# Optimization experiments

Measured on AMD Instinct MI355X. Metric: run time of the kernel, lower is better.

Reference implementation:

```python
import jax, jax.numpy as jnp
import numpy as np

N, E, D, M, R, NH, HD, FF = 20000, 160000, 64, 4, 5, 4, 16, 16


def _ln(x, g, b, eps=1e-5):
    mu = x.mean(-1, keepdims=True)
    var = ((x - mu) ** 2).mean(-1, keepdims=True)
    return (x - mu) / jnp.sqrt(var + eps) * g + b


def _encoder(x, p):
    # Post-norm nn.TransformerEncoderLayer(D, nhead=4, dim_feedforward=16), eval mode.
    # x: (B, 4, D); returns CLS output (B, D). Padding mask is all-zeros -> no masking.
    B = x.shape[0]
    qkv = x @ p['in_w'].T + p['in_b']                     # (B,4,3D)
    q, k, v = jnp.split(qkv, 3, axis=-1)
    hview = lambda t: t.reshape(B, 4, NH, HD).transpose(0, 2, 1, 3)  # (B,H,4,hd)
    q, k, v = hview(q), hview(k), hview(v)
    attn = jax.nn.softmax(jnp.einsum('bhqd,bhkd->bhqk', q, k) / jnp.sqrt(jnp.float32(HD)), axis=-1)
    o = jnp.einsum('bhqk,bhkd->bhqd', attn, v).transpose(0, 2, 1, 3).reshape(B, 4, D)
    o = o @ p['out_w'].T + p['out_b']
    x = _ln(x + o, p['ln1_g'], p['ln1_b'])
    ff = jax.nn.relu(x @ p['ff1_w'].T + p['ff1_b']) @ p['ff2_w'].T + p['ff2_b']
    x = _ln(x + ff, p['ln2_g'], p['ln2_b'])
    return x[:, 0, :]


def _mem_encode(h_a, h_b, cls_w, sep, p):
    # For each memory slot m: encode [CLS_m, h_a, SEP, h_b]; sum CLS outputs.
    B = h_a.shape[0]
    sep_t = jnp.broadcast_to(sep, (B, 1, D))
    outs = []
    mem_emb = jnp.zeros((B, D), h_a.dtype)
    for m in range(M):  # small fixed loop over memory slots
        cls_t = jnp.broadcast_to(cls_w[m], (B, 1, D))
        seq = jnp.concatenate([cls_t, h_a[:, None, :], sep_t, h_b[:, None, :]], axis=1)
        t = _encoder(seq, p)
        outs.append(t)
        mem_emb = mem_emb + t
    return mem_emb, outs


def setup_inputs() -> dict:
    key = jax.random.key(0)
    ks = jax.random.split(key, 16)
    s = 0.05
    f32 = jnp.float32
    inp = {}
    inp['feat'] = jax.random.normal(ks[0], (N, D), f32)
    inp['src'] = jax.random.randint(ks[1], (E,), 0, N, dtype=jnp.int32)
    inp['dst'] = jax.random.randint(ks[2], (E,), 0, N, dtype=jnp.int32)
    inp['etype'] = jax.random.randint(ks[3], (E,), 0, R, dtype=jnp.int32)
    inp['cls_w'] = jax.random.normal(ks[4], (M, D), f32)           # CLS embedding, std=1 as in source
    inp['sep'] = jax.random.normal(ks[5], (D,), f32)
    inp['in_w'] = jax.random.normal(ks[6], (3 * D, D), f32) * s
    inp['in_b'] = jnp.zeros((3 * D,), f32)
    inp['out_w'] = jax.random.normal(ks[7], (D, D), f32) * s
    inp['out_b'] = jnp.zeros((D,), f32)
    inp['ln1_g'] = jnp.ones((D,), f32)
    inp['ln1_b'] = jnp.zeros((D,), f32)
    inp['ln2_g'] = jnp.ones((D,), f32)
    inp['ln2_b'] = jnp.zeros((D,), f32)
    inp['ff1_w'] = jax.random.normal(ks[8], (FF, D), f32) * s
    inp['ff1_b'] = jnp.zeros((FF,), f32)
    inp['ff2_w'] = jax.random.normal(ks[9], (D, FF), f32) * s
    inp['ff2_b'] = jnp.zeros((D,), f32)
    inp['memcat_w'] = jax.random.normal(ks[10], (M, D), f32) * s
    inp['memcat_b'] = jnp.zeros((M,), f32)
    inp['memw_w'] = jax.random.normal(ks[11], (D * D, D), f32) * s
    inp['h_bias'] = jnp.zeros((D,), f32)
    inp['lnw_g'] = jnp.ones((D,), f32)
    inp['lnw_b'] = jnp.zeros((D,), f32)
    return inp


def reference(feat, src, dst, etype, cls_w, sep, in_w, in_b, out_w, out_b,
              ln1_g, ln1_b, ln2_g, ln2_b, ff1_w, ff1_b, ff2_w, ff2_b,
              memcat_w, memcat_b, memw_w, h_bias, lnw_g, lnw_b):
    p = dict(in_w=in_w, in_b=in_b, out_w=out_w, out_b=out_b, ln1_g=ln1_g, ln1_b=ln1_b,
             ln2_g=ln2_g, ln2_b=ln2_b, ff1_w=ff1_w, ff1_b=ff1_b, ff2_w=ff2_w, ff2_b=ff2_b)
    h_src = feat[src]                                      # (E,D) gather
    h_dst = feat[dst]
    # Per-etype loop in the source uses identical params for every edge, so the message
    # math vectorizes over all edges; only category/label ordering depends on etype.
    mem_emb, outs = _mem_encode(h_src, h_dst, cls_w, sep, p)   # (E,D)
    cat_all = jnp.stack([t @ memcat_w.T + memcat_b for t in outs])  # (M,E,mem_size)
    # Reproduce source ordering: for etype e (ascending), for slot m, edges in original order.
    counts = jnp.bincount(etype, length=R)
    start = jnp.cumsum(counts) - counts                    # exclusive prefix
    perm = jnp.argsort(etype)                              # stable sort by etype
    e_s = etype[perm]
    local = jnp.arange(E) - start[e_s]
    pos = M * start[e_s][None, :] + jnp.arange(M)[:, None] * counts[e_s][None, :] + local[None, :]  # (M,E)
    category = jnp.zeros((M * E, M), cat_all.dtype).at[pos.reshape(-1)].set(cat_all[:, perm].reshape(M * E, M))
    label = jnp.zeros((M * E,), jnp.int32).at[pos.reshape(-1)].set(
        jnp.broadcast_to(jnp.arange(M, dtype=jnp.int32)[:, None], (M, E)).reshape(-1))
    # Dynamic per-edge weight + message
    w = (mem_emb @ memw_w.T).reshape(-1, D, D)             # (E, out, in)
    msg = jnp.einsum('eoi,ei->eo', w, h_src)               # (E,D)
    # fn.mean aggregation (zero-degree nodes -> 0, matching DGL)
    deg = jax.ops.segment_sum(jnp.ones((E,), feat.dtype), dst, num_segments=N)
    agg = jax.ops.segment_sum(msg, dst, num_segments=N) / jnp.maximum(deg, 1.0)[:, None]
    node = _ln(agg, lnw_g, lnw_b) + h_bias
    # self-loop branch: same memory-slot transformer on (feat, feat)
    mem_emb_n, _ = _mem_encode(feat, feat, cls_w, sep, p)
    w_n = (mem_emb_n @ memw_w.T).reshape(-1, D, D)
    node = node + jnp.einsum('noi,ni->no', w_n, feat)
    node = jnp.where(node > 0, node, 0.2 * node)           # LeakyReLU(0.2); dropout is identity in eval
    return node, category, label
```

## Files before the change

kernel.cpp:

```cpp
#include <hip/hip_runtime.h>

#define DI __device__ __forceinline__

static constexpr int NN = 20000;
static constexpr int NE = 160000;

typedef __attribute__((ext_vector_type(4))) float f32x4;
typedef _Float16 f16x2 __attribute__((ext_vector_type(2)));
typedef _Float16 f16x8 __attribute__((ext_vector_type(8)));

DI float rl(float v, int lane) {
    return __int_as_float(__builtin_amdgcn_readlane(__float_as_int(v), lane));
}
DI float xr(float v, int m) { return __shfl_xor(v, m, 64); }
DI int xri(int v, int m) { return __shfl_xor(v, m, 64); }
DI float wsum64(float v) {
    v += xr(v, 1); v += xr(v, 2); v += xr(v, 4);
    v += xr(v, 8); v += xr(v, 16); v += xr(v, 32);
    return v;
}
DI int wsum64i(int v) {
    v += xri(v, 1); v += xri(v, 2); v += xri(v, 4);
    v += xri(v, 8); v += xri(v, 16); v += xri(v, 32);
    return v;
}
DI float hsum16(float v) {
    v += xr(v, 1); v += xr(v, 2); v += xr(v, 4); v += xr(v, 8);
    return v;
}
DI float hsum16d(float v) {
    v += __int_as_float(__builtin_amdgcn_mov_dpp(__float_as_int(v), 0xB1, 0xF, 0xF, true));
    v += __int_as_float(__builtin_amdgcn_mov_dpp(__float_as_int(v), 0x4E, 0xF, 0xF, true));
    v += __int_as_float(__builtin_amdgcn_mov_dpp(__float_as_int(v), 0x141, 0xF, 0xF, true));
    v += __int_as_float(__builtin_amdgcn_mov_dpp(__float_as_int(v), 0x140, 0xF, 0xF, true));
    return v;
}
DI float wsum64v(float v) {
    v = hsum16d(v);
    return (rl(v, 0) + rl(v, 16)) + (rl(v, 32) + rl(v, 48));
}
DI unsigned short f2h(float x) {
    union { _Float16 f; unsigned short u; } c;
    c.f = (_Float16)x;
    return c.u;
}

__global__ __launch_bounds__(256) void prepA_kernel(
    const float* __restrict__ mw, unsigned short* __restrict__ Wstg,
    const float* __restrict__ in_w, const float* __restrict__ out_w,
    float* __restrict__ WOVg,
    const float* __restrict__ cls_w, const float* __restrict__ sep,
    const float* __restrict__ in_b,
    const int* __restrict__ et, int* __restrict__ bc,
    float* __restrict__ agg, float* __restrict__ deg,
    const float* __restrict__ mc_w, const float* __restrict__ mc_b,
    const float* __restrict__ ln1_g, const float* __restrict__ ln1_b,
    const float* __restrict__ ln2_g, const float* __restrict__ ln2_b,
    const float* __restrict__ ff1_w, const float* __restrict__ ff1_b,
    const float* __restrict__ out_b,
    float* __restrict__ SWg, float* __restrict__ SB16,
    float* __restrict__ OvcG, float* __restrict__ OvsG,
    float* __restrict__ bOvG, float* __restrict__ s0n,
    float* __restrict__ s2n, float* __restrict__ MC8,
    float* __restrict__ GcT, float* __restrict__ GsT,
    float* __restrict__ DCC, float* __restrict__ B0T,
    float* __restrict__ mgT) {
    int b = blockIdx.x, t = threadIdx.x;
    __shared__ int c[5];
    __shared__ float P[608];
    if (b < 1024) {
        int idx = b * 256 + t;
        int d = idx & 63, o = (idx >> 6) & 63, i = idx >> 12;
        Wstg[idx] = f2h(mw[(o * 64 + i) * 64 + d]);
    } else if (b < 1088) {
        int u = (b - 1024) * 256 + t;
        int h = u & 3, l = (u >> 2) & 63, j = u >> 8;
        float acc = 0.f;
        for (int i = 0; i < 16; i++)
            acc += out_w[l * 64 + h * 16 + i] * in_w[(128 + h * 16 + i) * 64 + j];
        WOVg[u] = acc;
    } else if (b == 1088) {
        if (t < 64) {
            int l = t;
            float bq = in_b[l], bk = in_b[64 + l], bv = in_b[128 + l];
            float xs = sep[l];
            float ks = bk, vs = bv;
            for (int j = 0; j < 64; j++) {
                float xj = rl(xs, j);
                ks += in_w[(64 + l) * 64 + j] * xj;
                vs += in_w[(128 + l) * 64 + j] * xj;
            }
            P[512 + l] = vs;
            for (int m = 0; m < 4; m++) {
                float xc = cls_w[m * 64 + l];
                float q0 = bq, kc = bk, vc = bv;
                for (int j = 0; j < 64; j++) {
                    float xj = rl(xc, j);
                    q0 += in_w[l * 64 + j] * xj;
                    kc += in_w[(64 + l) * 64 + j] * xj;
                    vc += in_w[(128 + l) * 64 + j] * xj;
                }
                P[m * 64 + l] = q0;
                P[256 + m * 64 + l] = vc;
                float p0 = hsum16(q0 * kc);
                float p2 = hsum16(q0 * ks);
                if ((l & 15) == 0) {
                    P[576 + m * 4 + (l >> 4)] = p0 * 0.25f;
                    P[592 + m * 4 + (l >> 4)] = p2 * 0.25f;
                }
            }
        }
        __syncthreads();
        for (int u = t; u < 1024; u += 256) {
            int m = u >> 8, h = (u >> 6) & 3, j = u & 63;
            float acc = 0.f;
            for (int i = 0; i < 16; i++)
                acc += P[m * 64 + h * 16 + i] * in_w[(64 + h * 16 + i) * 64 + j];
            SWg[u] = 0.25f * acc;
        }
        for (int u = t; u < 1024; u += 256) {
            int h = u & 3, ll = (u >> 2) & 63, m = u >> 8;
            float acc = 0.f;
            for (int i = 0; i < 16; i++)
                acc += out_w[ll * 64 + h * 16 + i] * P[256 + m * 64 + h * 16 + i];
            OvcG[u] = acc;
        }
        if (t < 256) {
            int h = t & 3, ll = t >> 2;
            float a1 = 0.f, a2 = 0.f;
            for (int i = 0; i < 16; i++) {
                a1 += out_w[ll * 64 + h * 16 + i] * P[512 + h * 16 + i];
                a2 += out_w[ll * 64 + h * 16 + i] * in_b[128 + h * 16 + i];
            }
            OvsG[t] = a1;
            bOvG[t] = a2;
        }
        if (t < 256) {
            B0T[t] = cls_w[t] + out_b[t & 63];
            int p = t >> 2, cc = t & 3;
            mgT[t] = mc_w[cc * 64 + p] * ln2_g[p];
        }
        if (t < 16) {
            int m = t >> 2, h = t & 3;
            float acc = 0.f;
            for (int i = 0; i < 16; i++)
                acc += P[m * 64 + h * 16 + i] * in_b[64 + h * 16 + i];
            SB16[t] = 0.25f * acc;
            s0n[t] = P[576 + t];
            s2n[t] = P[592 + t];
        }
        if (t < 8) {
            int cc = t & 3;
            float acc = 0.f;
            if (t < 4) {
                for (int ll = 0; ll < 64; ll++) acc += mc_w[cc * 64 + ll] * ln2_g[ll];
            } else {
                for (int ll = 0; ll < 64; ll++) acc += mc_w[cc * 64 + ll] * ln2_b[ll];
                acc += mc_b[cc];
            }
            MC8[t] = acc;
        }
        __syncthreads();
        if (t < 256) {
            int m = t >> 6, f = (t >> 2) & 15, h = t & 3;
            float acc = 0.f;
            for (int p = 0; p < 64; p++)
                acc += ff1_w[f * 64 + p] * ln1_g[p] * OvcG[(m * 64 + p) * 4 + h];
            GcT[t] = acc;
        }
        if (t < 64) {
            int f = t >> 2, h = t & 3;
            float acc = 0.f;
            for (int p = 0; p < 64; p++)
                acc += ff1_w[f * 64 + p] * ln1_g[p] * OvsG[p * 4 + h];
            GsT[t] = acc;
        }
        if (t < 64) {
            int m = t >> 4, f = t & 15;
            float d0 = 0.f, c1 = 0.f, c2 = 0.f;
            for (int p = 0; p < 64; p++) {
                float wv = ff1_w[f * 64 + p];
                d0 += wv * ln1_g[p] * (cls_w[m * 64 + p] + out_b[p]);
                c1 += wv * ln1_g[p];
                c2 += wv * ln1_b[p];
            }
            f32x4 r = {d0, c1, c2 + ff1_b[f], 0.f};
            ((f32x4*)DCC)[t] = r;
        }
    } else if (b < 1714) {
        int bb = b - 1089;
        if (t < 5) c[t] = 0;
        __syncthreads();
        int e = bb * 256 + t;
        atomicAdd(&c[et[e]], 1);
        __syncthreads();
        if (t < 5) bc[bb * 5 + t] = c[t];
    } else if (b < 2964) {
        int idx = (b - 1714) * 256 + t;
        f32x4 z = {0.f, 0.f, 0.f, 0.f};
        ((f32x4*)agg)[idx] = z;
    } else {
        int idx = (b - 2964) * 256 + t;
        if (idx < 5000) {
            f32x4 z = {0.f, 0.f, 0.f, 0.f};
            ((f32x4*)deg)[idx] = z;
        }
    }
}

__global__ __launch_bounds__(256) void prepC_kernel(
    const int* __restrict__ et, const int* __restrict__ bc,
    const int* __restrict__ dstp, float* __restrict__ deg,
    int* __restrict__ rowbase, int* __restrict__ estride,
    const float* __restrict__ feat, const float* __restrict__ SWg,
    const float* __restrict__ SB16, const float* __restrict__ WOVg,
    const float* __restrict__ bOvG, const float* __restrict__ ff1_w,
    const float* __restrict__ ln1_g,
    float* __restrict__ Sout, float* __restrict__ Ovout, float* __restrict__ Gn) {
    __shared__ float SWs[1024];
    __shared__ f32x4 WOVs[4096];
    __shared__ __align__(16) float F1gL[1024];
    __shared__ __align__(16) float accT[4][4][64];
    __shared__ int wc[4][5];
    __shared__ int pre_s[5], tot_s[5], cs5[5];
    int tid = threadIdx.x;
    if (blockIdx.x < 625) {
        int b = blockIdx.x;
        if (tid < 5) { pre_s[tid] = 0; tot_s[tid] = 0; }
        __syncthreads();
#pragma unroll
        for (int ty = 0; ty < 5; ty++) {
            int pp = 0, tt = 0;
            for (int b2 = tid; b2 < 625; b2 += 256) {
                int v = bc[b2 * 5 + ty];
                tt += v;
                if (b2 < b) pp += v;
            }
            pp = wsum64i(pp);
            tt = wsum64i(tt);
            if ((tid & 63) == 0) {
                atomicAdd(&pre_s[ty], pp);
                atomicAdd(&tot_s[ty], tt);
            }
        }
        __syncthreads();
        if (tid == 0) {
            int s = 0;
            for (int e = 0; e < 5; e++) { cs5[e] = s; s += tot_s[e]; }
        }
        int w = tid >> 6, lane = tid & 63;
        int e = b * 256 + tid;
        int my = et[e];
        unsigned long long bal[5];
#pragma unroll
        for (int ty = 0; ty < 5; ty++) bal[ty] = __ballot(my == ty);
        if (lane == 0) {
#pragma unroll
            for (int ty = 0; ty < 5; ty++) wc[w][ty] = __popcll(bal[ty]);
        }
        __syncthreads();
        unsigned long long lt = ((unsigned long long)1 << lane) - 1;
        int intra = __popcll(bal[my] & lt);
        int pre = 0;
        for (int w2 = 0; w2 < w; w2++) pre += wc[w2][my];
        rowbase[e] = 4 * cs5[my] + pre_s[my] + pre + intra;
        estride[e] = tot_s[my];
        atomicAdd(&deg[dstp[e]], 1.0f);
        return;
    }
    int nb4 = blockIdx.x - 625;
    for (int p = tid; p < 1024; p += 256) {
        SWs[p] = SWg[p];
        F1gL[p] = ff1_w[p] * ln1_g[p & 63];
    }
    for (int p = tid; p < 4096; p += 256) WOVs[p] = ((const f32x4*)WOVg)[p];
    __syncthreads();
    int w = tid >> 6, l = tid & 63;
    int n = nb4 * 4 + w;
    float f = feat[(size_t)n * 64 + l];
    f32x4 acc = ((const f32x4*)bOvG)[l];
#pragma unroll 8
    for (int j = 0; j < 64; j++) {
        float fj = rl(f, j);
        f32x4 wv = WOVs[j * 64 + l];
        acc += wv * fj;
    }
    ((f32x4*)Ovout)[(size_t)n * 64 + l] = acc;
    accT[w][0][l] = acc[0];
    accT[w][1][l] = acc[1];
    accT[w][2][l] = acc[2];
    accT[w][3][l] = acc[3];
#pragma unroll
    for (int mh = 0; mh < 16; mh++) {
        float v = SWs[mh * 64 + l] * f;
        v = wsum64v(v);
        if (l == mh) Sout[(size_t)n * 16 + mh] = v + SB16[mh];
    }
    asm volatile("s_waitcnt lgkmcnt(0)" ::: "memory");
    int ff = l & 15, hh = l >> 4;
    float g = 0.f;
#pragma unroll
    for (int c2 = 0; c2 < 16; c2++) {
        int cc = (c2 + ff) & 15;
        f32x4 wv = *(const f32x4*)&F1gL[ff * 64 + cc * 4];
        f32x4 av = *(const f32x4*)&accT[w][hh][cc * 4];
        g += wv[0] * av[0] + wv[1] * av[1] + wv[2] * av[2] + wv[3] * av[3];
    }
    Gn[(size_t)n * 64 + ff * 4 + hh] = g;
}

__global__ __launch_bounds__(256, 4) void enc_kernel(
    const int* __restrict__ src, const int* __restrict__ dst,
    const float* __restrict__ Sg, const float* __restrict__ Ovg,
    const float* __restrict__ Gn, const float* __restrict__ OvcG,
    const float* __restrict__ OvsG, const float* __restrict__ GcT,
    const float* __restrict__ GsT, const float* __restrict__ DCC,
    const float* __restrict__ B0T, const float* __restrict__ mgT,
    const float* __restrict__ s0n, const float* __restrict__ s2n,
    const float* __restrict__ MC8,
    const float* __restrict__ ln1_g, const float* __restrict__ ln1_b,
    const float* __restrict__ ln2_g, const float* __restrict__ ln2_b,
    const float* __restrict__ ff2_w, const float* __restrict__ ff2_b,
    const int* __restrict__ rowbase, const int* __restrict__ estride,
    float* __restrict__ mem_out, float* __restrict__ out_cat,
    float* __restrict__ out_label) {
    __shared__ __align__(16) float F2C[1024];
    __shared__ __align__(16) float TBL[1704];
    int tid = threadIdx.x;
    for (int p = tid; p < 1024; p += 256) F2C[(p & 15) * 64 + (p >> 4)] = ff2_w[p];
    {
        f32x4* T4w = (f32x4*)TBL;
        int i = tid;
        if (i < 64) {
            T4w[i]        = ((const f32x4*)B0T)[i];
            T4w[64 + i]   = ((const f32x4*)GcT)[i];
            T4w[128 + i]  = ((const f32x4*)DCC)[i];
            T4w[192 + (i & 3) * 16 + (i >> 2)] = ((const f32x4*)OvsG)[i];
            T4w[256 + (i & 3) * 16 + (i >> 2)] = ((const f32x4*)mgT)[i];
        }
        if (i < 16) {
            T4w[320 + i] = ((const f32x4*)GsT)[i];
            T4w[346 + i] = *(const f32x4*)(ln1_g + i * 4);
            T4w[362 + i] = *(const f32x4*)(ln1_b + i * 4);
            T4w[378 + i] = *(const f32x4*)(ln2_g + i * 4);
            T4w[394 + i] = *(const f32x4*)(ln2_b + i * 4);
            T4w[410 + i] = *(const f32x4*)(ff2_b + i * 4);
        }
        if (i < 4) {
            T4w[336 + i] = ((const f32x4*)s0n)[i];
            T4w[340 + i] = ((const f32x4*)s2n)[i];
        }
        if (i < 2) T4w[344 + i] = ((const f32x4*)MC8)[i];
    }
    __syncthreads();
    const f32x4* F2C4 = (const f32x4*)F2C;
    const f32x4* Sg4 = (const f32x4*)Sg;
    const f32x4* Og4 = (const f32x4*)Ovg;
    const f32x4* Gn4 = (const f32x4*)Gn;

    int l = tid & 63, m = l >> 4, u = l & 15;
    f32x4 OvcR0 = ((const f32x4*)OvcG)[m * 64 + u * 4 + 0];
    f32x4 OvcR1 = ((const f32x4*)OvcG)[m * 64 + u * 4 + 1];
    f32x4 OvcR2 = ((const f32x4*)OvcG)[m * 64 + u * 4 + 2];
    f32x4 OvcR3 = ((const f32x4*)OvcG)[m * 64 + u * 4 + 3];
    int ubase = u * 17;
    int wid = blockIdx.x * 4 + (tid >> 6);
    int nw = gridDim.x * 4;

#pragma unroll 2
    for (int it = wid; it < NE + NN; it += nw) {
        int tb = 0;
        asm volatile("" : "+v"(tb));
        const f32x4* T4 = ((const f32x4*)TBL) + tb;
        int itu = __builtin_amdgcn_readfirstlane(it);
        bool isE = itu < NE;
        int ia = isE ? src[itu] : (itu - NE);
        f32x4 SaV = Sg4[(size_t)ia * 4 + m];
        f32x4 GaV = Gn4[(size_t)ia * 16 + u];
        f32x4 OvaR0 = Og4[(size_t)ia * 64 + u * 4 + 0];
        f32x4 OvaR1 = Og4[(size_t)ia * 64 + u * 4 + 1];
        f32x4 OvaR2 = Og4[(size_t)ia * 64 + u * 4 + 2];
        f32x4 OvaR3 = Og4[(size_t)ia * 64 + u * 4 + 3];
        f32x4 SbV = SaV, GbV = GaV;
        f32x4 OvbR0 = OvaR0, OvbR1 = OvaR1, OvbR2 = OvaR2, OvbR3 = OvaR3;
        int rb = 0, st = 0;
        if (isE) {
            int ib = dst[itu];
            SbV = Sg4[(size_t)ib * 4 + m];
            GbV = Gn4[(size_t)ib * 16 + u];
            OvbR0 = Og4[(size_t)ib * 64 + u * 4 + 0];
            OvbR1 = Og4[(size_t)ib * 64 + u * 4 + 1];
            OvbR2 = Og4[(size_t)ib * 64 + u * 4 + 2];
            OvbR3 = Og4[(size_t)ib * 64 + u * 4 + 3];
            rb = rowbase[itu];
            st = estride[itu];
        }
        f32x4 s0v = T4[336 + m];
        f32x4 s2v = T4[340 + m];
        f32x4 B0v = T4[l];
        f32x4 GcV = T4[64 + l];
        f32x4 DCv = T4[128 + l];
        f32x4 GsV = T4[320 + u];
        f32x4 OvsR0 = T4[192 + u];
        f32x4 OvsR1 = T4[208 + u];
        f32x4 OvsR2 = T4[224 + u];
        f32x4 OvsR3 = T4[240 + u];

        f32x4 mx, e0, e1, e2, e3, w0v, w1v, w2v, w3v;
#pragma unroll
        for (int h = 0; h < 4; h++)
            mx[h] = fmaxf(fmaxf(s0v[h], SaV[h]), fmaxf(s2v[h], SbV[h]));
#pragma unroll
        for (int h = 0; h < 4; h++) {
            e0[h] = __expf(s0v[h] - mx[h]);
            e1[h] = __expf(SaV[h] - mx[h]);
            e2[h] = __expf(s2v[h] - mx[h]);
            e3[h] = __expf(SbV[h] - mx[h]);
        }
#pragma unroll
        for (int h = 0; h < 4; h++) {
            float inv = 1.f / (e0[h] + e1[h] + e2[h] + e3[h]);
            w0v[h] = e0[h] * inv; w1v[h] = e1[h] * inv;
            w2v[h] = e2[h] * inv; w3v[h] = e3[h] * inv;
        }
        f32x4 xv = B0v;
#pragma unroll
        for (int h = 0; h < 4; h++) {
            float W0 = w0v[h], W1 = w1v[h], W2 = w2v[h], W3 = w3v[h];
            xv[0] += W0 * OvcR0[h] + W1 * OvaR0[h] + W2 * OvsR0[h] + W3 * OvbR0[h];
            xv[1] += W0 * OvcR1[h] + W1 * OvaR1[h] + W2 * OvsR1[h] + W3 * OvbR1[h];
            xv[2] += W0 * OvcR2[h] + W1 * OvaR2[h] + W2 * OvsR2[h] + W3 * OvbR2[h];
            xv[3] += W0 * OvcR3[h] + W1 * OvaR3[h] + W2 * OvsR3[h] + W3 * OvbR3[h];
        }
        float sx = hsum16d(xv[0] + xv[1] + xv[2] + xv[3]);
        float sxx = hsum16d(xv[0] * xv[0] + xv[1] * xv[1] + xv[2] * xv[2] + xv[3] * xv[3]);
        float mu = sx * 0.015625f;
        float var = sxx * 0.015625f - mu * mu;
        float r1 = rsqrtf(var + 1e-5f);
        f32x4 av = w0v * GcV + w1v * GaV + w2v * GsV + w3v * GbV;
        float accF = av[0] + av[1] + av[2] + av[3] + DCv[0];
        float hp = r1 * accF - (r1 * mu) * DCv[1] + DCv[2];
        float hr = fmaxf(hp, 0.f);
        f32x4 g1r = T4[346 + u], b1r = T4[362 + u], f2br = T4[410 + u];
        xv = (xv - mu) * (g1r * r1) + b1r;
        f32x4 yv = xv + f2br;
        float hrot = hr;
        int a16 = ubase + tb;
        { f32x4 wv = F2C4[a16]; yv += wv * hrot; }
#define FSTEP(CTL, MSK)                                                                         \
        hrot = __int_as_float(__builtin_amdgcn_mov_dpp(__float_as_int(hrot), (CTL), 0xF, 0xF, true)); \
        a16 ^= (MSK) * 16;                                                                      \
        { f32x4 wv = F2C4[a16]; yv += wv * hrot; }
        FSTEP(0xB1, 1) FSTEP(0x4E, 2) FSTEP(0xB1, 1) FSTEP(0x141, 7)
        FSTEP(0xB1, 1) FSTEP(0x4E, 2) FSTEP(0xB1, 1) FSTEP(0x140, 15)
        FSTEP(0xB1, 1) FSTEP(0x4E, 2) FSTEP(0xB1, 1) FSTEP(0x141, 7)
        FSTEP(0xB1, 1) FSTEP(0x4E, 2) FSTEP(0xB1, 1)
#undef FSTEP
        float sy = hsum16d(yv[0] + yv[1] + yv[2] + yv[3]);
        float syy = hsum16d(yv[0] * yv[0] + yv[1] * yv[1] + yv[2] * yv[2] + yv[3] * yv[3]);
        float mu2 = sy * 0.015625f;
        float var2 = syy * 0.015625f - mu2 * mu2;
        float r2 = rsqrtf(var2 + 1e-5f);
        f32x4 g2r = T4[378 + u], b2r = T4[394 + u];
        f32x4 tv = (yv - mu2) * (g2r * r2) + b2r;
        f32x4 mem4;
#pragma unroll
        for (int k = 0; k < 4; k++) {
            float s = tv[k];
            s += xr(s, 16);
            s += xr(s, 32);
            mem4[k] = s;
        }
        if (m == 0) *(f32x4*)(mem_out + (size_t)itu * 64 + u * 4) = mem4;
        if (isE) {
            f32x4 mg0 = T4[256 + u];
            f32x4 mg1 = T4[272 + u];
            f32x4 mg2 = T4[288 + u];
            f32x4 mg3 = T4[304 + u];
            f32x4 pcv = yv[0] * mg0 + yv[1] * mg1 + yv[2] * mg2 + yv[3] * mg3;
            f32x4 McV = T4[344];
            f32x4 CcV = T4[345];
            f32x4 dv;
            dv[0] = hsum16d(pcv[0]);
            dv[1] = hsum16d(pcv[1]);
            dv[2] = hsum16d(pcv[2]);
            dv[3] = hsum16d(pcv[3]);
            f32x4 cv = (dv - McV * mu2) * r2 + CcV;
            int row = rb + m * st;
            if (u == 0) {
                *(f32x4*)(out_cat + (size_t)row * 4) = cv;
                out_label[row] = (float)m;
            }
        }
    }
}

__global__ __launch_bounds__(256, 3) void msg_kernel(
    const float* __restrict__ feat, const int* __restrict__ src, const int* __restrict__ dstv,
    const float* __restrict__ mem_all, const unsigned short* __restrict__ Wstg,
    float* __restrict__ agg, float* __restrict__ msg_n) {
    constexpr int EB = NE / 256;
    int tid = threadIdx.x;
    int w = tid >> 6, lane = tid & 63;
    int m16 = lane & 15, q = lane >> 4;
    bool isE = blockIdx.x < EB;
    int blockbase = (isE ? blockIdx.x : blockIdx.x - EB) * 256;
    int count = isE ? NE : NN;
    size_t moff = isE ? 0 : (size_t)NE;
    int wavebase = w * 64;

    f16x2 mpk[4][2][4];
#pragma unroll
    for (int Mt = 0; Mt < 4; Mt++) {
        int it = blockbase + wavebase + Mt * 16 + m16;
        if (!isE && it >= count) it = count - 1;
        const float* mrow = mem_all + (moff + (size_t)it) * 64;
#pragma unroll
        for (int ks = 0; ks < 2; ks++) {
            float4 a = *(const float4*)(mrow + ks * 32 + q * 8);
            float4 b = *(const float4*)(mrow + ks * 32 + q * 8 + 4);
            mpk[Mt][ks][0] = f16x2{(_Float16)a.x, (_Float16)a.y};
            mpk[Mt][ks][1] = f16x2{(_Float16)a.z, (_Float16)a.w};
            mpk[Mt][ks][2] = f16x2{(_Float16)b.x, (_Float16)b.y};
            mpk[Mt][ks][3] = f16x2{(_Float16)b.z, (_Float16)b.w};
        }
    }
    f32x4 acc[4][4];
#pragma unroll
    for (int Mt = 0; Mt < 4; Mt++)
#pragma unroll
        for (int nt = 0; nt < 4; nt++) {
            f32x4 z = {0.f, 0.f, 0.f, 0.f};
            acc[Mt][nt] = z;
        }

    int hit = blockbase + tid;
    if (!isE && hit >= count) hit = count - 1;
    int hidx = isE ? src[hit] : hit;
    const float* hrow = feat + (size_t)hidx * 64;

    for (int ch = 0; ch < 16; ch++) {
        float4 hv = *(const float4*)(hrow + ch * 4);
        unsigned hpk[4];
        {
            union { f16x2 f; unsigned u; } cc;
            cc.f = f16x2{(_Float16)hv.x, (_Float16)hv.x}; hpk[0] = cc.u;
            cc.f = f16x2{(_Float16)hv.y, (_Float16)hv.y}; hpk[1] = cc.u;
            cc.f = f16x2{(_Float16)hv.z, (_Float16)hv.z}; hpk[2] = cc.u;
            cc.f = f16x2{(_Float16)hv.w, (_Float16)hv.w}; hpk[3] = cc.u;
        }
#pragma unroll
        for (int il = 0; il < 4; il++) {
            const unsigned short* wtile = Wstg + (size_t)(ch * 4 + il) * 4096;
            f16x8 afr[4][2];
#pragma unroll
            for (int Mt = 0; Mt < 4; Mt++) {
                union { f16x2 f; unsigned u; } hh;
                hh.u = (unsigned)__shfl((int)hpk[il], Mt * 16 + m16, 64);
                f16x2 hd = hh.f;
#pragma unroll
                for (int ks = 0; ks < 2; ks++) {
                    union { unsigned u[4]; f16x8 v; } uu;
#pragma unroll
                    for (int jj = 0; jj < 4; jj++) {
                        union { f16x2 f; unsigned u; } rr;
                        rr.f = mpk[Mt][ks][jj] * hd;
                        uu.u[jj] = rr.u;
                    }
                    afr[Mt][ks] = uu.v;
                }
            }
#pragma unroll
            for (int nt = 0; nt < 4; nt++) {
                int o = nt * 16 + m16;
#pragma unroll
                for (int ks = 0; ks < 2; ks++) {
                    union { uint4 u; f16x8 v; } bb;
                    bb.u = *(const uint4*)&wtile[o * 64 + ks * 32 + q * 8];
#pragma unroll
                    for (int Mt = 0; Mt < 4; Mt++)
                        acc[Mt][nt] = __builtin_amdgcn_mfma_f32_16x16x32_f16(
                            afr[Mt][ks], bb.v, acc[Mt][nt], 0, 0, 0);
                }
            }
        }
    }
#pragma unroll
    for (int Mt = 0; Mt < 4; Mt++) {
        int ib = blockbase + wavebase + Mt * 16 + q * 4;
        if (!isE) {
#pragma unroll
            for (int r = 0; r < 4; r++) {
                int it = ib + r;
                if (it < count) {
#pragma unroll
                    for (int nt = 0; nt < 4; nt++)
                        msg_n[(size_t)it * 64 + nt * 16 + m16] = acc[Mt][nt][r];
                }
            }
        } else {
            int4 dd = *(const int4*)(dstv + ib);
#pragma unroll
            for (int r = 0; r < 4; r++) {
                int dn = (&dd.x)[r];
#pragma unroll
                for (int nt = 0; nt < 4; nt++)
                    atomicAdd(&agg[(size_t)dn * 64 + nt * 16 + m16], acc[Mt][nt][r]);
            }
        }
    }
}

__global__ __launch_bounds__(256) void final_kernel(
    const float* __restrict__ agg, const float* __restrict__ deg, const float* __restrict__ msgn,
    const float* __restrict__ lnw_g, const float* __restrict__ lnw_b,
    const float* __restrict__ h_bias, float* __restrict__ outp, int nN) {
    int tid = threadIdx.x, w = tid >> 6, l = tid & 63;
    int n = blockIdx.x * 4 + w;
    if (n >= nN) return;
    float a = agg[(size_t)n * 64 + l] / fmaxf(deg[n], 1.f);
    float mu = wsum64(a) * (1.f / 64.f);
    float d = a - mu;
    float var = wsum64(d * d) * (1.f / 64.f);
    float v = d * rsqrtf(var + 1e-5f) * lnw_g[l] + lnw_b[l] + h_bias[l] + msgn[(size_t)n * 64 + l];
    outp[(size_t)n * 64 + l] = v > 0.f ? v : 0.2f * v;
}


extern "C" void kernel_launch(void* const* d_in, const int* in_sizes, int n_in,
                              void* d_out, int out_size, void* d_ws, size_t ws_size,
                              hipStream_t stream) {
    const float* feat   = (const float*)d_in[0];
    const int*   src    = (const int*)d_in[1];
    const int*   dst    = (const int*)d_in[2];
    const int*   etype  = (const int*)d_in[3];
    const float* cls_w  = (const float*)d_in[4];
    const float* sep    = (const float*)d_in[5];
    const float* in_w   = (const float*)d_in[6];
    const float* in_b   = (const float*)d_in[7];
    const float* out_w  = (const float*)d_in[8];
    const float* out_b  = (const float*)d_in[9];
    const float* ln1_g  = (const float*)d_in[10];
    const float* ln1_b  = (const float*)d_in[11];
    const float* ln2_g  = (const float*)d_in[12];
    const float* ln2_b  = (const float*)d_in[13];
    const float* ff1_w  = (const float*)d_in[14];
    const float* ff1_b  = (const float*)d_in[15];
    const float* ff2_w  = (const float*)d_in[16];
    const float* ff2_b  = (const float*)d_in[17];
    const float* mc_w   = (const float*)d_in[18];
    const float* mc_b   = (const float*)d_in[19];
    const float* memw_w = (const float*)d_in[20];
    const float* h_bias = (const float*)d_in[21];
    const float* lnw_g  = (const float*)d_in[22];
    const float* lnw_b  = (const float*)d_in[23];

    char* ws = (char*)d_ws;
    size_t off = 0;
    auto nxt = [&](size_t bytes) -> void* {
        void* p = ws + off;
        off += (bytes + 255) & ~(size_t)255;
        return p;
    };
    unsigned short* Wstg = (unsigned short*)nxt(64 * 64 * 64 * sizeof(unsigned short));
    float* SWg     = (float*)nxt(1024 * sizeof(float));
    float* SB16    = (float*)nxt(16 * sizeof(float));
    float* OvcG    = (float*)nxt(1024 * sizeof(float));
    float* OvsG    = (float*)nxt(256 * sizeof(float));
    float* bOvG    = (float*)nxt(256 * sizeof(float));
    float* s0n     = (float*)nxt(16 * sizeof(float));
    float* s2n     = (float*)nxt(16 * sizeof(float));
    float* MC8     = (float*)nxt(8 * sizeof(float));
    float* GcT     = (float*)nxt(256 * sizeof(float));
    float* GsT     = (float*)nxt(64 * sizeof(float));
    float* DCC     = (float*)nxt(256 * sizeof(float));
    float* B0T     = (float*)nxt(256 * sizeof(float));
    float* mgT     = (float*)nxt(256 * sizeof(float));
    float* WOVg    = (float*)nxt(16384 * sizeof(float));
    float* Sg      = (float*)nxt((size_t)NN * 16 * sizeof(float));
    float* Ovg     = (float*)nxt((size_t)NN * 256 * sizeof(float));
    float* Gn      = (float*)nxt((size_t)NN * 64 * sizeof(float));
    int*   bc      = (int*)nxt(625 * 5 * sizeof(int));
    int*   rowbase = (int*)nxt((size_t)NE * sizeof(int));
    int*   estride = (int*)nxt((size_t)NE * sizeof(int));
    float* mem_all = (float*)nxt((size_t)(NE + NN) * 64 * sizeof(float));
    float* agg     = (float*)nxt((size_t)NN * 64 * sizeof(float));
    float* deg     = (float*)nxt((size_t)NN * sizeof(float));
    float* msg_n   = (float*)nxt((size_t)NN * 64 * sizeof(float));
    (void)ws_size; (void)in_sizes; (void)n_in; (void)out_size;

    float* out_node  = (float*)d_out;
    float* out_cat   = out_node + (size_t)NN * 64;
    float* out_label = out_cat + (size_t)4 * NE * 4;

    prepA_kernel<<<2984, 256, 0, stream>>>(
        memw_w, Wstg, in_w, out_w, WOVg, cls_w, sep, in_b, etype, bc, agg, deg,
        mc_w, mc_b, ln1_g, ln1_b, ln2_g, ln2_b, ff1_w, ff1_b, out_b,
        SWg, SB16, OvcG, OvsG, bOvG, s0n, s2n, MC8, GcT, GsT, DCC, B0T, mgT);
    prepC_kernel<<<5625, 256, 0, stream>>>(etype, bc, dst, deg, rowbase, estride,
                                           feat, SWg, SB16, WOVg, bOvG, ff1_w, ln1_g,
                                           Sg, Ovg, Gn);
    enc_kernel<<<2048, 256, 0, stream>>>(
        src, dst, Sg, Ovg, Gn, OvcG, OvsG, GcT, GsT, DCC, B0T, mgT, s0n, s2n, MC8,
        ln1_g, ln1_b, ln2_g, ln2_b, ff2_w, ff2_b,
        rowbase, estride, mem_all, out_cat, out_label);
    msg_kernel<<<625 + (NN + 255) / 256, 256, 0, stream>>>(
        feat, src, dst, mem_all, Wstg, agg, msg_n);

    final_kernel<<<(NN + 3) / 4, 256, 0, stream>>>(agg, deg, msg_n, lnw_g, lnw_b, h_bias, out_node, NN);
}
```

Measured before the change: 631.2 us.

## Stage per-chunk weight tiles in padded LDS with register prefetch in msg_kernel

```diff
diff --git a/kernel.cpp b/kernel.cpp
--- a/kernel.cpp
+++ b/kernel.cpp
@@ -495,11 +495,13 @@
     }
 }
 
-__global__ __launch_bounds__(256, 3) void msg_kernel(
+__global__ __launch_bounds__(256, 2) void msg_kernel(
     const float* __restrict__ feat, const int* __restrict__ src, const int* __restrict__ dstv,
     const float* __restrict__ mem_all, const unsigned short* __restrict__ Wstg,
     float* __restrict__ agg, float* __restrict__ msg_n) {
+    constexpr int RS = 72;
     constexpr int EB = NE / 256;
+    __shared__ __align__(16) unsigned short Wt[4 * 64 * RS];
     int tid = threadIdx.x;
     int w = tid >> 6, lane = tid & 63;
     int m16 = lane & 15, q = lane >> 4;
@@ -539,7 +541,25 @@
     int hidx = isE ? src[hit] : hit;
     const float* hrow = feat + (size_t)hidx * 64;
 
+    uint4 stg[8];
+#pragma unroll
+    for (int p = 0; p < 8; p++)
+        stg[p] = *(const uint4*)(Wstg + p * 2048 + tid * 8);
+#pragma unroll
+    for (int p = 0; p < 8; p++) {
+        int flat = p * 2048 + tid * 8;
+        int ic = flat >> 12, o = (flat >> 6) & 63, d = flat & 63;
+        *(uint4*)&Wt[(ic * 64 + o) * RS + d] = stg[p];
+    }
+    __syncthreads();
+
     for (int ch = 0; ch < 16; ch++) {
+        if (ch < 15) {
+            const unsigned short* gsl = Wstg + (size_t)(ch + 1) * 16384;
+#pragma unroll
+            for (int p = 0; p < 8; p++)
+                stg[p] = *(const uint4*)(gsl + p * 2048 + tid * 8);
+        }
         float4 hv = *(const float4*)(hrow + ch * 4);
         unsigned hpk[4];
         {
@@ -551,7 +571,6 @@
         }
 #pragma unroll
         for (int il = 0; il < 4; il++) {
-            const unsigned short* wtile = Wstg + (size_t)(ch * 4 + il) * 4096;
             f16x8 afr[4][2];
 #pragma unroll
             for (int Mt = 0; Mt < 4; Mt++) {
@@ -570,19 +589,30 @@
                     afr[Mt][ks] = uu.v;
                 }
             }
+            const unsigned short* wrow = &Wt[(il * 64) * RS];
 #pragma unroll
             for (int nt = 0; nt < 4; nt++) {
                 int o = nt * 16 + m16;
 #pragma unroll
                 for (int ks = 0; ks < 2; ks++) {
                     union { uint4 u; f16x8 v; } bb;
-                    bb.u = *(const uint4*)&wtile[o * 64 + ks * 32 + q * 8];
+                    bb.u = *(const uint4*)&wrow[o * RS + ks * 32 + q * 8];
 #pragma unroll
                     for (int Mt = 0; Mt < 4; Mt++)
                         acc[Mt][nt] = __builtin_amdgcn_mfma_f32_16x16x32_f16(
                             afr[Mt][ks], bb.v, acc[Mt][nt], 0, 0, 0);
                 }
             }
+        }
+        __syncthreads();
+        if (ch < 15) {
+#pragma unroll
+            for (int p = 0; p < 8; p++) {
+                int flat = p * 2048 + tid * 8;
+                int ic = flat >> 12, o = (flat >> 6) & 63, d = flat & 63;
+                *(uint4*)&Wt[(ic * 64 + o) * RS + d] = stg[p];
+            }
+            __syncthreads();
         }
     }
 #pragma unroll
```

After: 605.6 us. -4.0%, faster.
